# Performance work log

Measured on AMD Instinct MI355X. Metric: run time of the kernel, lower is better.

The kernel has to match this reference:

```python
import jax, jax.numpy as jnp
import numpy as np

NUM_Q, NUM_P = 64, 1024


def setup_inputs() -> dict:
    key = jax.random.key(0)
    k1, k2 = jax.random.split(key)
    pred = jax.random.normal(k1, (NUM_Q, NUM_P), dtype=jnp.float32)
    y = (jax.random.uniform(k2, (NUM_Q, NUM_P)) < 0.1).astype(jnp.float32)
    return {"pred": pred, "y": y}


def reference(pred, y):
    # Original: for each query i, for each relevant index j (y[i,j]==1),
    # MarginRankingLoss(sum)(x1=pred[i,j].repeat(P), x2=pred[i], target=(y[i]!=1))
    # with margin=0: per-element loss = max(0, -t*(x1-x2)).
    #   t=0 (relevant k):     max(0, 0) = 0
    #   t=1 (non-relevant k): max(0, pred[i,k] - pred[i,j])
    # => loss[i] = sum_{j: rel} sum_{k: non-rel} relu(pred[i,k] - pred[i,j])
    # result = loss.mean() over queries. (bce branch disabled in config.)
    rel = (y == 1.0)                       # [Q,P] relevant mask (j axis)
    neg = ~rel                             # [Q,P] non-relevant mask (k axis)
    # diff[i,j,k] = pred[i,k] - pred[i,j]
    diff = pred[:, None, :] - pred[:, :, None]          # [Q,P,P]
    pair_mask = rel[:, :, None] & neg[:, None, :]       # [Q,P,P]
    hinge = jnp.where(pair_mask, jnp.maximum(diff, 0.0), 0.0)
    loss = jnp.sum(hinge, axis=(1, 2))                  # [Q]
    return jnp.mean(loss)
```

## Files before the change

### kernel.cpp

```cpp
#include <hip/hip_runtime.h>
#include <math.h>

#define NUM_Q 64
#define NUM_P 1024
#define BLOCK 1024
#define NPAD  1028

__global__ __launch_bounds__(BLOCK) void per_query_loss_kernel(
    const float* __restrict__ pred,
    const float* __restrict__ y,
    float* __restrict__ out)
{
    __shared__ __align__(16) float relVals[NPAD];
    __shared__ int   relCount;
    __shared__ float waveSums[BLOCK / 64];

    const int q    = blockIdx.x;
    const int tid  = threadIdx.x;
    const int wave = tid >> 6;
    const int lane = tid & 63;

    if (tid == 0) atomicCAS((unsigned int*)out, 0xAAAAAAAAu, 0u);

    const float* __restrict__ prow = pred + q * NUM_P;
    const float* __restrict__ yrow = y    + q * NUM_P;

    for (int i = tid; i < NPAD; i += BLOCK) relVals[i] = INFINITY;
    if (tid == 0) relCount = 0;
    __syncthreads();

    const float p  = prow[tid];
    const float yy = yrow[tid];
    const bool rel = (yy == 1.0f);

    const unsigned long long mask = __ballot(rel);
    const int waveRel = __popcll(mask);
    int waveBase = 0;
    if (lane == 0 && waveRel) waveBase = atomicAdd(&relCount, waveRel);
    waveBase = __shfl(waveBase, 0, 64);
    if (rel) {
        const int pos = waveBase +
            __popcll(mask & ((1ull << lane) - 1ull));
        relVals[pos] = p;
    }
    const float mp = rel ? -INFINITY : p;
    __syncthreads();

    const int nChunks = (relCount + 3) >> 2;
    const float4* __restrict__ rv4 = (const float4*)relVals;

    float a0 = 0.0f, a1 = 0.0f, a2 = 0.0f, a3 = 0.0f;
    #pragma unroll 2
    for (int c = 0; c < nChunks; ++c) {
        const float4 rv = rv4[c];
        a0 += fmaxf(mp - rv.x, 0.0f);
        a1 += fmaxf(mp - rv.y, 0.0f);
        a2 += fmaxf(mp - rv.z, 0.0f);
        a3 += fmaxf(mp - rv.w, 0.0f);
    }
    float acc = (a0 + a1) + (a2 + a3);

    #pragma unroll
    for (int off = 32; off > 0; off >>= 1)
        acc += __shfl_down(acc, off, 64);
    if (lane == 0) waveSums[wave] = acc;
    __syncthreads();

    if (wave == 0) {
        float v = (lane < BLOCK / 64) ? waveSums[lane] : 0.0f;
        #pragma unroll
        for (int off = 8; off > 0; off >>= 1)
            v += __shfl_down(v, off, 64);
        if (lane == 0)
            atomicAdd(out, v * (1.0f / NUM_Q));
    }
}

extern "C" void kernel_launch(void* const* d_in, const int* in_sizes, int n_in,
                              void* d_out, int out_size, void* d_ws, size_t ws_size,
                              hipStream_t stream) {
    const float* pred = (const float*)d_in[0];
    const float* y    = (const float*)d_in[1];
    float* out = (float*)d_out;

    per_query_loss_kernel<<<NUM_Q, BLOCK, 0, stream>>>(pred, y, out);
}
```

Measured before the change: 58.16 us.

## Split each query across four blocks and vectorize row loads

Launches four 256-thread blocks per query instead of one 1024-thread block, so the 64 queries are spread over 256 workgroups rather than 64. Each block loads the whole row with float4 loads and builds the full list of relevant scores using four ballots per wave. It then accumulates hinge terms only for its own quarter of the non-relevant elements, chosen by the lane component. The cost is that every block repeats the row load and relevant-list compaction, and four times as many blocks issue atomics on the output.

```diff
diff --git a/kernel.cpp b/kernel.cpp
--- a/kernel.cpp
+++ b/kernel.cpp
@@ -3,7 +3,8 @@
 
 #define NUM_Q 64
 #define NUM_P 1024
-#define BLOCK 1024
+#define BLOCK 256
+#define SPLIT 4
 #define NPAD  1028
 
 __global__ __launch_bounds__(BLOCK) void per_query_loss_kernel(
@@ -15,35 +16,48 @@
     __shared__ int   relCount;
     __shared__ float waveSums[BLOCK / 64];
 
-    const int q    = blockIdx.x;
+    const int q    = blockIdx.x >> 2;
+    const int s    = blockIdx.x & 3;
     const int tid  = threadIdx.x;
     const int wave = tid >> 6;
     const int lane = tid & 63;
 
     if (tid == 0) atomicCAS((unsigned int*)out, 0xAAAAAAAAu, 0u);
 
-    const float* __restrict__ prow = pred + q * NUM_P;
-    const float* __restrict__ yrow = y    + q * NUM_P;
+    const float4* __restrict__ prow4 = (const float4*)(pred + q * NUM_P);
+    const float4* __restrict__ yrow4 = (const float4*)(y    + q * NUM_P);
+
+    const float4 p4 = prow4[tid];
+    const float4 y4 = yrow4[tid];
 
     for (int i = tid; i < NPAD; i += BLOCK) relVals[i] = INFINITY;
     if (tid == 0) relCount = 0;
     __syncthreads();
 
-    const float p  = prow[tid];
-    const float yy = yrow[tid];
-    const bool rel = (yy == 1.0f);
+    const bool r0 = (y4.x == 1.0f), r1 = (y4.y == 1.0f);
+    const bool r2 = (y4.z == 1.0f), r3 = (y4.w == 1.0f);
+    const unsigned long long m0 = __ballot(r0);
+    const unsigned long long m1 = __ballot(r1);
+    const unsigned long long m2 = __ballot(r2);
+    const unsigned long long m3 = __ballot(r3);
+    const int c0 = __popcll(m0), c1 = __popcll(m1);
+    const int c2 = __popcll(m2), c3 = __popcll(m3);
+    const int total = c0 + c1 + c2 + c3;
+    int base = 0;
+    if (lane == 0 && total) base = atomicAdd(&relCount, total);
+    base = __shfl(base, 0, 64);
+    const unsigned long long lt = (1ull << lane) - 1ull;
+    if (r0) relVals[base                + __popcll(m0 & lt)] = p4.x;
+    if (r1) relVals[base + c0           + __popcll(m1 & lt)] = p4.y;
+    if (r2) relVals[base + c0 + c1      + __popcll(m2 & lt)] = p4.z;
+    if (r3) relVals[base + c0 + c1 + c2 + __popcll(m3 & lt)] = p4.w;
 
-    const unsigned long long mask = __ballot(rel);
-    const int waveRel = __popcll(mask);
-    int waveBase = 0;
-    if (lane == 0 && waveRel) waveBase = atomicAdd(&relCount, waveRel);
-    waveBase = __shfl(waveBase, 0, 64);
-    if (rel) {
-        const int pos = waveBase +
-            __popcll(mask & ((1ull << lane) - 1ull));
-        relVals[pos] = p;
-    }
-    const float mp = rel ? -INFINITY : p;
+    float pe, ye;
+    if      (s == 0) { pe = p4.x; ye = y4.x; }
+    else if (s == 1) { pe = p4.y; ye = y4.y; }
+    else if (s == 2) { pe = p4.z; ye = y4.z; }
+    else             { pe = p4.w; ye = y4.w; }
+    const float mp = (ye == 1.0f) ? -INFINITY : pe;
     __syncthreads();
 
     const int nChunks = (relCount + 3) >> 2;
@@ -68,9 +82,8 @@
 
     if (wave == 0) {
         float v = (lane < BLOCK / 64) ? waveSums[lane] : 0.0f;
-        #pragma unroll
-        for (int off = 8; off > 0; off >>= 1)
-            v += __shfl_down(v, off, 64);
+        v += __shfl_down(v, 2, 64);
+        v += __shfl_down(v, 1, 64);
         if (lane == 0)
             atomicAdd(out, v * (1.0f / NUM_Q));
     }
@@ -83,5 +96,5 @@
     const float* y    = (const float*)d_in[1];
     float* out = (float*)d_out;
 
-    per_query_loss_kernel<<<NUM_Q, BLOCK, 0, stream>>>(pred, y, out);
+    per_query_loss_kernel<<<NUM_Q * SPLIT, BLOCK, 0, stream>>>(pred, y, out);
 }
```

Result: slower. 60.45 us (+3.9%).
